# Kernel optimization log

Hardware: AMD Instinct MI355X
Metric: run time of the kernel (lower is better)

Reference implementation:

```python
import jax, jax.numpy as jnp
import numpy as np

SCALE = 100.0

def _build_tables():
    b2n = np.zeros((256, 32), np.float32)
    n2b = np.zeros((32, 256), np.float32)
    for byte in range(256):
        h, l = byte >> 4, byte & 15
        b2n[byte, h] = 1.0
        b2n[byte, 16 + l] = 1.0
        n2b[h, byte] = 1.0
        n2b[16 + l, byte] = 1.0
    add_table = np.zeros((16, 16, 2, 16), np.float32)
    carry_table = np.zeros((16, 16, 2, 2), np.float32)
    for x in range(16):
        for y in range(16):
            for c in range(2):
                t = x + y + c
                add_table[x, y, c, t % 16] = 1.0
                carry_table[x, y, c, t // 16] = 1.0
    return b2n, n2b, add_table, carry_table

def setup_inputs() -> dict:
    key = jax.random.key(0)
    k1, k2 = jax.random.split(key)
    B = 32768
    a = jax.random.normal(k1, (B, 4, 256), dtype=jnp.float32)
    b = jax.random.normal(k2, (B, 4, 256), dtype=jnp.float32)
    b2n, n2b, add_table, carry_table = _build_tables()
    return {"a": a, "b": b,
            "b2n": jnp.asarray(b2n), "n2b": jnp.asarray(n2b),
            "add_table": jnp.asarray(add_table), "carry_table": jnp.asarray(carry_table)}

def _byte_add_single(a, b, b2n, n2b, add_table, carry_table):
    # a, b: [4, 256]
    def to_nibbles(x):
        comb = x @ b2n  # [32]
        return jax.nn.softmax(comb[:16] * SCALE), jax.nn.softmax(comb[16:] * SCALE)

    def nibble_add(x, y, cin):
        # cin has shape [1] initially (broadcasts over carry axis, as torch einsum does) or [2]
        w = x[:, None, None] * y[None, :, None] * cin[None, None, :]
        w = jnp.broadcast_to(w, (16, 16, 2))
        s = jnp.einsum('ijk,ijkl->l', w, add_table)
        c = jnp.einsum('ijk,ijkl->l', w, carry_table)
        return jax.nn.softmax(s * SCALE), jax.nn.softmax(c * SCALE)

    def from_nibbles(h, l):
        return jax.nn.softmax((jnp.concatenate([h, l]) @ n2b) * SCALE)

    carry = jnp.ones((1,), a.dtype)  # matches torch.tensor([1.0]) initial carry
    outs = []
    for i in range(4):  # fixed 4-byte carry chain
        ah, al = to_nibbles(a[i])
        bh, bl = to_nibbles(b[i])
        sl, carry_out = nibble_add(al, bl, carry)
        sh, carry = nibble_add(ah, bh, carry_out)
        outs.append(from_nibbles(sh, sl))
    return jnp.stack(outs)  # [4, 256]

def reference(a, b, b2n, n2b, add_table, carry_table):
    f = jax.vmap(_byte_add_single, in_axes=(0, 0, None, None, None, None))
    return f(a, b, b2n, n2b, add_table, carry_table)  # [B, 4, 256]
```

## Files before the change

### kernel.cpp

```cpp
#include <hip/hip_runtime.h>
#include <cstddef>
#include <math.h>


__device__ __forceinline__ float exf(float t) {
  return (float)exp((double)t);
}

__device__ __forceinline__ void softmax16_np(const float* x, float* p) {
#pragma clang fp contract(off)
  float t[16];
#pragma unroll
  for (int j = 0; j < 16; ++j) t[j] = x[j] * 100.0f;
  float m = t[0];
#pragma unroll
  for (int j = 1; j < 16; ++j) m = fmaxf(m, t[j]);
  float e[16];
#pragma unroll
  for (int j = 0; j < 16; ++j) e[j] = exf(t[j] - m);
  float r0 = e[0] + e[8], r1 = e[1] + e[9], r2 = e[2] + e[10], r3 = e[3] + e[11];
  float r4 = e[4] + e[12], r5 = e[5] + e[13], r6 = e[6] + e[14], r7 = e[7] + e[15];
  float s = ((r0 + r1) + (r2 + r3)) + ((r4 + r5) + (r6 + r7));
#pragma unroll
  for (int j = 0; j < 16; ++j) p[j] = e[j] / s;
}

__device__ __forceinline__ void nibble_add_raw(const float* px, const float* py,
                                               float c0, float c1,
                                               float* s, float& n0, float& n1) {
#pragma clang fp contract(off)
  float ca = 0.f, cb = 0.f;
#pragma unroll
  for (int l = 0; l < 16; ++l) s[l] = 0.f;
#pragma unroll
  for (int i = 0; i < 16; ++i) {
#pragma unroll
    for (int j = 0; j < 16; ++j) {
      float wij = px[i] * py[j];
      float w0 = wij * c0;
      float w1 = wij * c1;
      const int t0 = i + j, t1 = i + j + 1;
      s[t0 & 15] += w0;
      if (t0 < 16) ca += w0; else cb += w0;
      s[t1 & 15] += w1;
      if (t1 < 16) ca += w1; else cb += w1;
    }
  }
  float u0 = ca * 100.0f, u1 = cb * 100.0f;
  float m = fmaxf(u0, u1);
  float e0 = exf(u0 - m), e1 = exf(u1 - m);
  float ss = e0 + e1;
  n0 = e0 / ss;
  n1 = e1 / ss;
}

extern "C" __global__ void __launch_bounds__(256, 4)
k1_prep(const float* __restrict__ A, const float* __restrict__ Bm,
        float* __restrict__ ws1, int nbatch) {
#pragma clang fp contract(off)
  __shared__ float buf[32][261];
  __shared__ float comb[32][33];
  const int tid = threadIdx.x;
  const int wave = tid >> 6, lane = tid & 63;
  const int batch0 = blockIdx.x * 32;
  const int ib = blockIdx.y, inp = blockIdx.z;
  if (batch0 >= nbatch) return;
  const float* __restrict__ src =
      (inp == 0 ? A : Bm) + (size_t)batch0 * 1024 + ib * 256;

#pragma unroll
  for (int it = 0; it < 8; ++it) {
    const int bb = it * 4 + wave;
    *(float4*)&buf[bb][lane * 4] =
        *(const float4*)(src + (size_t)bb * 1024 + lane * 4);
  }
  __syncthreads();

  {
    const int g = tid >> 5;
    const int bb = tid & 31;
    if (g < 4) {
#pragma unroll
      for (int q = 0; q < 4; ++q) {
        const int u = g * 4 + q;
        float a = 0.f;
#pragma unroll
        for (int e = 0; e < 16; ++e) a += buf[bb][u * 16 + e];
        comb[bb][u] = a;
      }
    } else {
#pragma unroll
      for (int q = 0; q < 4; ++q) {
        const int l = (g - 4) * 4 + q;
        float a = 0.f;
#pragma unroll
        for (int m = 0; m < 16; ++m) a += buf[bb][m * 16 + l];
        comb[bb][16 + l] = a;
      }
    }
  }
  __syncthreads();

  if (tid < 64) {
    const int bb = tid & 31, nib = tid >> 5;
    float x[16], p[16];
#pragma unroll
    for (int j = 0; j < 16; ++j) x[j] = comb[bb][nib * 16 + j];
    softmax16_np(x, p);
    const size_t r0 = (size_t)((ib * 2 + inp) * 32 + nib * 16);
#pragma unroll
    for (int j = 0; j < 16; ++j)
      ws1[(r0 + j) * nbatch + batch0 + bb] = p[j];
  }
}

__device__ __forceinline__ void k2_load(const float* __restrict__ ws1, int i,
                                        size_t batch, int nbatch, float* b) {
#pragma unroll
  for (int t = 0; t < 64; ++t)
    b[t] = ws1[(size_t)(i * 64 + t) * nbatch + batch];
}

__device__ __forceinline__ void k2_step(const float* b, float& cr0, float& cr1,
                                        float* __restrict__ ws2, int i,
                                        size_t batch, int nbatch) {
  float sl[16], sh[16], d0, d1;
  nibble_add_raw(b + 16, b + 48, cr0, cr1, sl, d0, d1);
  nibble_add_raw(b + 0,  b + 32, d0, d1, sh, cr0, cr1);
#pragma unroll
  for (int l = 0; l < 16; ++l) {
    ws2[(size_t)(i * 32 + l) * nbatch + batch] = sh[l];
    ws2[(size_t)(i * 32 + 16 + l) * nbatch + batch] = sl[l];
  }
}

extern "C" __global__ void __launch_bounds__(64, 1)
k2_chain(const float* __restrict__ ws1, float* __restrict__ ws2, int nbatch) {
  const size_t batch = (size_t)blockIdx.x * 64 + threadIdx.x;
  if (batch >= (size_t)nbatch) return;
  float cr0 = 1.0f, cr1 = 1.0f;
  float bufA[64], bufB[64];
  k2_load(ws1, 0, batch, nbatch, bufA);
  k2_load(ws1, 1, batch, nbatch, bufB);
  k2_step(bufA, cr0, cr1, ws2, 0, batch, nbatch);
  k2_load(ws1, 2, batch, nbatch, bufA);
  k2_step(bufB, cr0, cr1, ws2, 1, batch, nbatch);
  k2_load(ws1, 3, batch, nbatch, bufB);
  k2_step(bufA, cr0, cr1, ws2, 2, batch, nbatch);
  k2_step(bufB, cr0, cr1, ws2, 3, batch, nbatch);
}

extern "C" __global__ void __launch_bounds__(256, 4)
k3_out(const float* __restrict__ ws2, float* __restrict__ O, int nbatch) {
  __shared__ float pout[2][64][36];
  const int tid = threadIdx.x;
  const int batch0 = blockIdx.x * 64;
  const int ib0 = blockIdx.y * 2;
  if (batch0 >= nbatch) return;

  {
    const int ibl = tid >> 7;
    const int nib = (tid >> 6) & 1;
    const int bb = tid & 63;
    float x[16], p[16], p2[16];
#pragma unroll
    for (int l = 0; l < 16; ++l)
      x[l] = ws2[(size_t)((ib0 + ibl) * 32 + nib * 16 + l) * nbatch + batch0 + bb];
    softmax16_np(x, p);
    softmax16_np(p, p2);
#pragma unroll
    for (int j = 0; j < 16; ++j) pout[ibl][bb][nib * 20 + j] = p2[j];
  }
  __syncthreads();

#pragma unroll
  for (int ibl = 0; ibl < 2; ++ibl) {
#pragma unroll
    for (int kk = 0; kk < 16; ++kk) {
      int flat = kk * 1024 + tid * 4;
      int bb = flat >> 8;
      int b0 = flat & 255;
      float ph = pout[ibl][bb][b0 >> 4];
      int lo = 20 + (b0 & 15);
      float4 o;
      o.x = ph * pout[ibl][bb][lo + 0];
      o.y = ph * pout[ibl][bb][lo + 1];
      o.z = ph * pout[ibl][bb][lo + 2];
      o.w = ph * pout[ibl][bb][lo + 3];
      *(float4*)(O + ((size_t)(batch0 + bb) * 4 + ib0 + ibl) * 256 + b0) = o;
    }
  }
}

__device__ __forceinline__ void nibble_add_np_fb(const float* px, const float* py,
                                                 float c0, float c1,
                                                 float* ps, float& n0, float& n1) {
  float s[16];
  nibble_add_raw(px, py, c0, c1, s, n0, n1);
  softmax16_np(s, ps);
}

__device__ __forceinline__ void buckets_np_fb(const float* __restrict__ row,
                                              float* hi, float* lo) {
#pragma clang fp contract(off)
#pragma unroll
  for (int j = 0; j < 16; ++j) { hi[j] = 0.f; lo[j] = 0.f; }
#pragma unroll
  for (int k4 = 0; k4 < 64; ++k4) {
    float4 x = *(const float4*)(row + k4 * 4);
    const int h = k4 >> 2, l0 = (k4 & 3) * 4;
    hi[h] += x.x;  hi[h] += x.y;  hi[h] += x.z;  hi[h] += x.w;
    lo[l0 + 0] += x.x;
    lo[l0 + 1] += x.y;
    lo[l0 + 2] += x.z;
    lo[l0 + 3] += x.w;
  }
}

extern "C" __global__ void __launch_bounds__(64, 1)
byteadd_fallback(const float* __restrict__ A, const float* __restrict__ Bm,
                 float* __restrict__ O, int nbatch) {
#pragma clang fp contract(off)
  const int b = blockIdx.x * 64 + threadIdx.x;
  if (b >= nbatch) return;
  const float* Ab = A + (size_t)b * 1024;
  const float* Bb = Bm + (size_t)b * 1024;
  float* Ob = O + (size_t)b * 1024;
  float cr0 = 1.0f, cr1 = 1.0f;
#pragma unroll 1
  for (int i = 0; i < 4; ++i) {
    float ah[16], al[16], bh[16], bl[16];
    buckets_np_fb(Ab + i * 256, ah, al);
    buckets_np_fb(Bb + i * 256, bh, bl);
    float pah[16], pal[16], pbh[16], pbl[16];
    softmax16_np(ah, pah);
    softmax16_np(al, pal);
    softmax16_np(bh, pbh);
    softmax16_np(bl, pbl);
    float psl[16], psh[16], d0, d1;
    nibble_add_np_fb(pal, pbl, cr0, cr1, psl, d0, d1);
    nibble_add_np_fb(pah, pbh, d0, d1, psh, cr0, cr1);
    float ph2[16], pl2[16];
    softmax16_np(psh, ph2);
    softmax16_np(psl, pl2);
#pragma unroll
    for (int k4 = 0; k4 < 64; ++k4) {
      const int h = k4 >> 2, l0 = (k4 & 3) * 4;
      const float ph = ph2[h];
      float4 o;
      o.x = ph * pl2[l0 + 0];
      o.y = ph * pl2[l0 + 1];
      o.z = ph * pl2[l0 + 2];
      o.w = ph * pl2[l0 + 3];
      *(float4*)(Ob + i * 256 + k4 * 4) = o;
    }
  }
}

extern "C" void kernel_launch(void* const* d_in, const int* in_sizes, int n_in,
                              void* d_out, int out_size, void* d_ws, size_t ws_size,
                              hipStream_t stream) {
  const float* A = (const float*)d_in[0];
  const float* B = (const float*)d_in[1];
  float* O = (float*)d_out;
  int nbatch = in_sizes[0] / 1024;
  size_t need = (size_t)384 * nbatch * sizeof(float);
  if (ws_size >= need && (nbatch & 63) == 0) {
    float* ws1 = (float*)d_ws;
    float* ws2 = ws1 + (size_t)256 * nbatch;
    k1_prep<<<dim3(nbatch / 32, 4, 2), dim3(256), 0, stream>>>(A, B, ws1, nbatch);
    k2_chain<<<dim3(nbatch / 64), dim3(64), 0, stream>>>(ws1, ws2, nbatch);
    k3_out<<<dim3(nbatch / 64, 2), dim3(256), 0, stream>>>(ws2, O, nbatch);
  } else {
    byteadd_fallback<<<dim3((nbatch + 63) / 64), dim3(64), 0, stream>>>(A, B, O, nbatch);
  }
}
```

Measured before the change: 196.6 us.

## Make k1_prep persistent over 8 chunks with register prefetch and batched softmax

Each k1_prep block now walks 8 consecutive 32-batch chunks instead of one. The next chunk's global loads go into registers while the current chunk's nibble sums are computed, and softmax runs on four chunks at once so all 256 threads take part. The change also adds an early return in exf for very negative inputs, so the double-precision exp is skipped, and lowers the launch-bounds occupancy hint. In exchange the grid is 8x smaller, fewer blocks are in flight to hide latency, register and LDS use go up, and the fast path now needs the batch count to be a multiple of 256.

```diff
diff --git a/kernel.cpp b/kernel.cpp
--- a/kernel.cpp
+++ b/kernel.cpp
@@ -4,6 +4,7 @@
 
 
 __device__ __forceinline__ float exf(float t) {
+  if (t < -104.0f) return 0.0f;
   return (float)exp((double)t);
 }
 
@@ -54,63 +55,82 @@
   n1 = e1 / ss;
 }
 
-extern "C" __global__ void __launch_bounds__(256, 4)
+extern "C" __global__ void __launch_bounds__(256, 3)
 k1_prep(const float* __restrict__ A, const float* __restrict__ Bm,
         float* __restrict__ ws1, int nbatch) {
 #pragma clang fp contract(off)
   __shared__ float buf[32][261];
-  __shared__ float comb[32][33];
+  __shared__ float comb4[128][33];
   const int tid = threadIdx.x;
   const int wave = tid >> 6, lane = tid & 63;
-  const int batch0 = blockIdx.x * 32;
   const int ib = blockIdx.y, inp = blockIdx.z;
-  if (batch0 >= nbatch) return;
-  const float* __restrict__ src =
-      (inp == 0 ? A : Bm) + (size_t)batch0 * 1024 + ib * 256;
-
-#pragma unroll
-  for (int it = 0; it < 8; ++it) {
-    const int bb = it * 4 + wave;
-    *(float4*)&buf[bb][lane * 4] =
-        *(const float4*)(src + (size_t)bb * 1024 + lane * 4);
+  const float* __restrict__ base = (inp == 0 ? A : Bm);
+  const int chunk0 = blockIdx.x * 8;
+
+  float4 regs[8];
+  {
+    const float* src = base + (size_t)chunk0 * 32 * 1024 + ib * 256;
+#pragma unroll
+    for (int it = 0; it < 8; ++it)
+      regs[it] = *(const float4*)(src + (size_t)(it * 4 + wave) * 1024 + lane * 4);
+#pragma unroll
+    for (int it = 0; it < 8; ++it)
+      *(float4*)&buf[it * 4 + wave][lane * 4] = regs[it];
   }
   __syncthreads();
 
-  {
-    const int g = tid >> 5;
-    const int bb = tid & 31;
-    if (g < 4) {
-#pragma unroll
-      for (int q = 0; q < 4; ++q) {
-        const int u = g * 4 + q;
-        float a = 0.f;
-#pragma unroll
-        for (int e = 0; e < 16; ++e) a += buf[bb][u * 16 + e];
-        comb[bb][u] = a;
+  for (int c = 0; c < 8; ++c) {
+    if (c + 1 < 8) {
+      const float* src = base + (size_t)(chunk0 + c + 1) * 32 * 1024 + ib * 256;
+#pragma unroll
+      for (int it = 0; it < 8; ++it)
+        regs[it] = *(const float4*)(src + (size_t)(it * 4 + wave) * 1024 + lane * 4);
+    }
+    {
+      const int g = tid >> 5, bb = tid & 31;
+      float* crow = &comb4[(c & 3) * 32 + bb][0];
+      if (g < 4) {
+#pragma unroll
+        for (int q = 0; q < 4; ++q) {
+          const int u = g * 4 + q;
+          float a = 0.f;
+#pragma unroll
+          for (int e = 0; e < 16; ++e) a += buf[bb][u * 16 + e];
+          crow[u] = a;
+        }
+      } else {
+#pragma unroll
+        for (int q = 0; q < 4; ++q) {
+          const int l = (g - 4) * 4 + q;
+          float a = 0.f;
+#pragma unroll
+          for (int m = 0; m < 16; ++m) a += buf[bb][m * 16 + l];
+          crow[16 + l] = a;
+        }
       }
-    } else {
-#pragma unroll
-      for (int q = 0; q < 4; ++q) {
-        const int l = (g - 4) * 4 + q;
-        float a = 0.f;
-#pragma unroll
-        for (int m = 0; m < 16; ++m) a += buf[bb][m * 16 + l];
-        comb[bb][16 + l] = a;
-      }
-    }
-  }
-  __syncthreads();
-
-  if (tid < 64) {
-    const int bb = tid & 31, nib = tid >> 5;
-    float x[16], p[16];
-#pragma unroll
-    for (int j = 0; j < 16; ++j) x[j] = comb[bb][nib * 16 + j];
-    softmax16_np(x, p);
-    const size_t r0 = (size_t)((ib * 2 + inp) * 32 + nib * 16);
-#pragma unroll
-    for (int j = 0; j < 16; ++j)
-      ws1[(r0 + j) * nbatch + batch0 + bb] = p[j];
+    }
+    __syncthreads();
+
+    if (c + 1 < 8) {
+#pragma unroll
+      for (int it = 0; it < 8; ++it)
+        *(float4*)&buf[it * 4 + wave][lane * 4] = regs[it];
+    }
+    if ((c & 3) == 3) {
+      const int cc = tid >> 6;
+      const int nib = (tid >> 5) & 1;
+      const int bb = tid & 31;
+      float x[16], p[16];
+#pragma unroll
+      for (int j = 0; j < 16; ++j) x[j] = comb4[cc * 32 + bb][nib * 16 + j];
+      softmax16_np(x, p);
+      const int batch = (chunk0 + (c & ~3) + cc) * 32 + bb;
+      const size_t r0 = (size_t)((ib * 2 + inp) * 32 + nib * 16);
+#pragma unroll
+      for (int j = 0; j < 16; ++j)
+        ws1[(r0 + j) * nbatch + batch] = p[j];
+    }
+    __syncthreads();
   }
 }
 
@@ -265,10 +285,10 @@
   float* O = (float*)d_out;
   int nbatch = in_sizes[0] / 1024;
   size_t need = (size_t)384 * nbatch * sizeof(float);
-  if (ws_size >= need && (nbatch & 63) == 0) {
+  if (ws_size >= need && (nbatch & 255) == 0) {
     float* ws1 = (float*)d_ws;
     float* ws2 = ws1 + (size_t)256 * nbatch;
-    k1_prep<<<dim3(nbatch / 32, 4, 2), dim3(256), 0, stream>>>(A, B, ws1, nbatch);
+    k1_prep<<<dim3(nbatch / 256, 4, 2), dim3(256), 0, stream>>>(A, B, ws1, nbatch);
     k2_chain<<<dim3(nbatch / 64), dim3(64), 0, stream>>>(ws1, ws2, nbatch);
     k3_out<<<dim3(nbatch / 64, 2), dim3(256), 0, stream>>>(ws2, O, nbatch);
   } else {
```

New measurement: 653.8 us. 3.33x slower.
